# Kernel tuning notes

Measured on AMD Instinct MI355X. Metric: run time of the kernel, lower is better.

The kernel has to match this reference:

```python
import jax, jax.numpy as jnp
import numpy as np

N = 100_000      # nodes
M = 200_000      # hyperedges
E = 1_000_000    # incidence pairs
D_IN = 64
HEADS, D_OUT = 8, 16   # linear out = 8*16 = 128


def setup_inputs() -> dict:
    key = jax.random.key(0)
    k = jax.random.split(key, 7)
    X = jax.random.normal(k[0], (N, D_IN), dtype=jnp.float32)
    vertex = jax.random.randint(k[1], (E,), 0, N, dtype=jnp.int32)
    edges = jax.random.randint(k[2], (E,), 0, M, dtype=jnp.int32)
    dege = jax.random.uniform(k[3], (M, 1), dtype=jnp.float32)
    degv = jax.random.uniform(k[4], (N, 1), dtype=jnp.float32)
    W = jax.random.normal(k[5], (D_IN, HEADS * D_OUT), dtype=jnp.float32) / np.sqrt(D_IN)
    b = jax.random.normal(k[6], (HEADS * D_OUT,), dtype=jnp.float32) * 0.01
    return {"X": X, "vertex": vertex, "edges": edges, "dege": dege, "degv": degv, "W": W, "b": b}


def reference(X, vertex, edges, dege, degv, W, b):
    n_nodes = X.shape[0]
    n_edges = dege.shape[0]
    # vertex -> hyperedge aggregation (first_aggregate = 'mean')
    Xve = X[vertex]                                               # [E, D]
    sums = jax.ops.segment_sum(Xve, edges, num_segments=n_edges)  # [M, D]
    counts = jax.ops.segment_sum(jnp.ones((edges.shape[0],), X.dtype), edges, num_segments=n_edges)
    Xe = sums / jnp.maximum(counts, 1.0)[:, None]                 # empty edges -> 0
    Xe = Xe * dege
    # hyperedge -> vertex aggregation (sum)
    Xev = Xe[edges]                                               # [E, D]
    Xv = jax.ops.segment_sum(Xev, vertex, num_segments=n_nodes)   # [N, D]
    Xv = Xv * degv
    # normalize_l2: row norm is computed on a DETACHED tensor in torch
    rownorm = jnp.linalg.norm(jax.lax.stop_gradient(Xv), axis=1, keepdims=True)
    scale = jnp.where(rownorm > 0, 1.0 / rownorm, 0.0)
    Xn = Xv * scale
    return Xn @ W + b
```

## Files before the change

### kernel.cpp

```cpp
#include <hip/hip_runtime.h>


#define DIN 64
#define DOUT 128
#define CH 4096
#define BSHIFT 9
#define FINE 512
#define PAYBITS 18
#define PAYMASK ((1u << PAYBITS) - 1u)
#define XB 256
#define STAGE 8192

typedef float f32x4 __attribute__((ext_vector_type(4)));
typedef short bf16x8 __attribute__((ext_vector_type(8)));

__device__ __forceinline__ unsigned short f2b(float f) {
  unsigned u = __float_as_uint(f);
  u = u + 0x7fffu + ((u >> 16) & 1u);
  return (unsigned short)(u >> 16);
}
__device__ __forceinline__ float b2f(unsigned s) {
  return __uint_as_float(s << 16);
}

__global__ __launch_bounds__(512) void k_p1(
    const int* __restrict__ vertex, const int* __restrict__ edges,
    int* __restrict__ G, const float* __restrict__ X,
    unsigned short* __restrict__ Xb, int* __restrict__ done,
    int E, int BKE, int BK, int NCH, int total4) {
  if (blockIdx.x == 0 && threadIdx.x == 0) *done = 0;
  if (blockIdx.x >= (unsigned)NCH) {
    int xb = blockIdx.x - NCH;
    for (int i = xb * 512 + threadIdx.x; i < total4; i += XB * 512) {
      float4 a = ((const float4*)X)[i];
      ushort4 r;
      r.x = f2b(a.x); r.y = f2b(a.y); r.z = f2b(a.z); r.w = f2b(a.w);
      ((ushort4*)Xb)[i] = r;
    }
    return;
  }
  __shared__ int h[1024];
  for (int i = threadIdx.x; i < BK; i += 512) h[i] = 0;
  __syncthreads();
  int c = blockIdx.x;
  int s = c * CH, e_ = min(E, s + CH);
  int n4 = (e_ - s) >> 2;
  const int4* ep = (const int4*)(edges + s);
  const int4* vp = (const int4*)(vertex + s);
  for (int i = threadIdx.x; i < n4; i += 512) {
    int4 ee = ep[i], vv = vp[i];
    atomicAdd(&h[ee.x >> BSHIFT], 1); atomicAdd(&h[ee.y >> BSHIFT], 1);
    atomicAdd(&h[ee.z >> BSHIFT], 1); atomicAdd(&h[ee.w >> BSHIFT], 1);
    atomicAdd(&h[BKE + (vv.x >> BSHIFT)], 1); atomicAdd(&h[BKE + (vv.y >> BSHIFT)], 1);
    atomicAdd(&h[BKE + (vv.z >> BSHIFT)], 1); atomicAdd(&h[BKE + (vv.w >> BSHIFT)], 1);
  }
  for (int i = s + (n4 << 2) + threadIdx.x; i < e_; i += 512) {
    atomicAdd(&h[edges[i] >> BSHIFT], 1);
    atomicAdd(&h[BKE + (vertex[i] >> BSHIFT)], 1);
  }
  __syncthreads();
  for (int b = threadIdx.x; b < BK; b += 512) G[(size_t)b * NCH + c] = h[b];
}

__global__ __launch_bounds__(256) void k_p1b(
    int* __restrict__ G, int* __restrict__ rowTot, int* __restrict__ bucketBase,
    int* __restrict__ done, int NCH, int BK) {
  int b = blockIdx.x;
  int* row = G + (size_t)b * NCH;
  __shared__ int wsum[4];
  __shared__ int carry;
  __shared__ bool amLast;
  if (threadIdx.x == 0) carry = 0;
  __syncthreads();
  for (int base = 0; base < NCH; base += 256) {
    int i = base + threadIdx.x;
    int v = (i < NCH) ? row[i] : 0;
    int lane = threadIdx.x & 63, wid = threadIdx.x >> 6;
    int inc = v;
    #pragma unroll
    for (int o = 1; o < 64; o <<= 1) {
      int t = __shfl_up(inc, o);
      if (lane >= o) inc += t;
    }
    if (lane == 63) wsum[wid] = inc;
    __syncthreads();
    int woff = carry;
    for (int w = 0; w < wid; ++w) woff += wsum[w];
    int excl = woff + inc - v;
    if (i < NCH) row[i] = excl;
    __syncthreads();
    if (threadIdx.x == 0) carry += wsum[0] + wsum[1] + wsum[2] + wsum[3];
    __syncthreads();
  }
  if (threadIdx.x == 0) {
    rowTot[b] = carry;
    __threadfence();
    amLast = (atomicAdd(done, 1) == gridDim.x - 1);
  }
  __syncthreads();
  if (!amLast) return;

  if (threadIdx.x == 0) carry = 0;
  __syncthreads();
  for (int base = 0; base < BK; base += 256) {
    int i = base + threadIdx.x;
    int v = (i < BK) ? atomicAdd(&rowTot[i], 0) : 0;
    int lane = threadIdx.x & 63, wid = threadIdx.x >> 6;
    int inc = v;
    #pragma unroll
    for (int o = 1; o < 64; o <<= 1) {
      int t = __shfl_up(inc, o);
      if (lane >= o) inc += t;
    }
    if (lane == 63) wsum[wid] = inc;
    __syncthreads();
    int woff = carry;
    for (int w = 0; w < wid; ++w) woff += wsum[w];
    int excl = woff + inc - v;
    if (i < BK) bucketBase[i] = excl;
    __syncthreads();
    if (threadIdx.x == 0) carry += wsum[0] + wsum[1] + wsum[2] + wsum[3];
    __syncthreads();
  }
  if (threadIdx.x == 0) bucketBase[BK] = carry;
}

__global__ __launch_bounds__(512) void p2_scatter(
    const int* __restrict__ vertex, const int* __restrict__ edges,
    const int* __restrict__ G, const int* __restrict__ bucketBase,
    unsigned* __restrict__ temp, int E, int BKE, int BK, int NCH) {
  __shared__ int curs[1024];
  int c = blockIdx.x;
  for (int b = threadIdx.x; b < BK; b += 512)
    curs[b] = bucketBase[b] + G[(size_t)b * NCH + c];
  __syncthreads();
  int s = c * CH, e_ = min(E, s + CH);
  int n4 = (e_ - s) >> 2;
  const int4* ep = (const int4*)(edges + s);
  const int4* vp = (const int4*)(vertex + s);
  for (int i = threadIdx.x; i < n4; i += 512) {
    int4 ee = ep[i], vv = vp[i];
    int p;
    p = atomicAdd(&curs[ee.x >> BSHIFT], 1);
    temp[p] = ((unsigned)(ee.x & (FINE - 1)) << PAYBITS) | (unsigned)vv.x;
    p = atomicAdd(&curs[BKE + (vv.x >> BSHIFT)], 1);
    temp[p] = ((unsigned)(vv.x & (FINE - 1)) << PAYBITS) | (unsigned)ee.x;
    p = atomicAdd(&curs[ee.y >> BSHIFT], 1);
    temp[p] = ((unsigned)(ee.y & (FINE - 1)) << PAYBITS) | (unsigned)vv.y;
    p = atomicAdd(&curs[BKE + (vv.y >> BSHIFT)], 1);
    temp[p] = ((unsigned)(vv.y & (FINE - 1)) << PAYBITS) | (unsigned)ee.y;
    p = atomicAdd(&curs[ee.z >> BSHIFT], 1);
    temp[p] = ((unsigned)(ee.z & (FINE - 1)) << PAYBITS) | (unsigned)vv.z;
    p = atomicAdd(&curs[BKE + (vv.z >> BSHIFT)], 1);
    temp[p] = ((unsigned)(vv.z & (FINE - 1)) << PAYBITS) | (unsigned)ee.z;
    p = atomicAdd(&curs[ee.w >> BSHIFT], 1);
    temp[p] = ((unsigned)(ee.w & (FINE - 1)) << PAYBITS) | (unsigned)vv.w;
    p = atomicAdd(&curs[BKE + (vv.w >> BSHIFT)], 1);
    temp[p] = ((unsigned)(vv.w & (FINE - 1)) << PAYBITS) | (unsigned)ee.w;
  }
  for (int i = s + (n4 << 2) + threadIdx.x; i < e_; i += 512) {
    int e = edges[i], v = vertex[i];
    int pE = atomicAdd(&curs[e >> BSHIFT], 1);
    temp[pE] = ((unsigned)(e & (FINE - 1)) << PAYBITS) | (unsigned)v;
    int pV = atomicAdd(&curs[BKE + (v >> BSHIFT)], 1);
    temp[pV] = ((unsigned)(v & (FINE - 1)) << PAYBITS) | (unsigned)e;
  }
}

__global__ __launch_bounds__(256) void p3_sort(
    const unsigned* __restrict__ temp, const int* __restrict__ bucketBase,
    int* __restrict__ off, int* __restrict__ perm, int BKE, int M, int N) {
  __shared__ int hist[FINE];
  __shared__ int pos[FINE];
  __shared__ int wsum[4];
  __shared__ unsigned pairsS[STAGE];
  int g = blockIdx.x;
  bool isE = g < BKE;
  int gg = isE ? g : g - BKE;
  int keyBase = gg << BSHIFT;
  int cap = isE ? M : N;
  int offBase = (isE ? 0 : M) + keyBase;
  int fineCount = min(FINE, cap - keyBase);
  int pairBase = bucketBase[g], pairEnd = bucketBase[g + 1];
  int cnt = pairEnd - pairBase;
  bool staged = cnt <= STAGE;

  for (int i = threadIdx.x; i < FINE; i += 256) hist[i] = 0;
  __syncthreads();
  if (staged) {
    for (int i = threadIdx.x; i < cnt; i += 256) {
      unsigned p = temp[pairBase + i];
      pairsS[i] = p;
      atomicAdd(&hist[p >> PAYBITS], 1);
    }
  } else {
    for (int i = threadIdx.x; i < cnt; i += 256)
      atomicAdd(&hist[temp[pairBase + i] >> PAYBITS], 1);
  }
  __syncthreads();

  int t2 = threadIdx.x * 2;
  int a0 = hist[t2], a1 = hist[t2 + 1];
  int tsum = a0 + a1;
  int lane = threadIdx.x & 63, wid = threadIdx.x >> 6;
  int inc = tsum;
  #pragma unroll
  for (int o = 1; o < 64; o <<= 1) {
    int t = __shfl_up(inc, o);
    if (lane >= o) inc += t;
  }
  if (lane == 63) wsum[wid] = inc;
  __syncthreads();
  int woff = 0;
  for (int w = 0; w < wid; ++w) woff += wsum[w];
  int excl = woff + inc - tsum;
  pos[t2] = excl; pos[t2 + 1] = excl + a0;
  __syncthreads();

  for (int f = threadIdx.x; f < fineCount; f += 256)
    off[offBase + f] = pairBase + pos[f] + hist[f];
  for (int f = threadIdx.x; f < FINE; f += 256) pos[f] += pairBase;
  __syncthreads();

  if (staged) {
    for (int i = threadIdx.x; i < cnt; i += 256) {
      unsigned p = pairsS[i];
      int q = atomicAdd(&pos[p >> PAYBITS], 1);
      perm[q] = (int)(p & PAYMASK);
    }
  } else {
    for (int i = threadIdx.x; i < cnt; i += 256) {
      unsigned p = temp[pairBase + i];
      int q = atomicAdd(&pos[p >> PAYBITS], 1);
      perm[q] = (int)(p & PAYMASK);
    }
  }
}


__global__ __launch_bounds__(256) void k_edge(
    const unsigned short* __restrict__ Xb, const int* __restrict__ off,
    const int* __restrict__ perm, const float* __restrict__ dege,
    unsigned short* __restrict__ Xe, int M) {
  long long gid = (long long)blockIdx.x * 256 + threadIdx.x;
  int wv = (int)(gid >> 6);
  int lane = threadIdx.x & 63;
  int g = lane >> 3, li = lane & 7;
  int e = wv * 8 + g;
  bool valid = e < M;
  int start = 0, end = 0;
  if (valid) { start = e ? off[e - 1] : 0; end = off[e]; }
  int deg = end - start;
  int myidx = (valid && li < deg) ? perm[start + li] : 0;
  int jmax = min(deg, 8);
  int jw = jmax;
  jw = max(jw, __shfl_xor(jw, 8));
  jw = max(jw, __shfl_xor(jw, 16));
  jw = max(jw, __shfl_xor(jw, 32));
  const uint4* X4 = (const uint4*)Xb;
  float acc[8] = {0.f, 0.f, 0.f, 0.f, 0.f, 0.f, 0.f, 0.f};
  #pragma unroll 4
  for (int j = 0; j < jw; ++j) {
    int v0 = __shfl(myidx, (g << 3) + j);
    if (j < jmax) {
      uint4 a = X4[(size_t)v0 * 8 + li];
      acc[0] += b2f(a.x & 0xffffu); acc[1] += b2f(a.x >> 16);
      acc[2] += b2f(a.y & 0xffffu); acc[3] += b2f(a.y >> 16);
      acc[4] += b2f(a.z & 0xffffu); acc[5] += b2f(a.z >> 16);
      acc[6] += b2f(a.w & 0xffffu); acc[7] += b2f(a.w >> 16);
    }
  }
  for (int j = 8; j < deg; ++j) {
    int v0 = perm[start + j];
    uint4 a = X4[(size_t)v0 * 8 + li];
    acc[0] += b2f(a.x & 0xffffu); acc[1] += b2f(a.x >> 16);
    acc[2] += b2f(a.y & 0xffffu); acc[3] += b2f(a.y >> 16);
    acc[4] += b2f(a.z & 0xffffu); acc[5] += b2f(a.z >> 16);
    acc[6] += b2f(a.w & 0xffffu); acc[7] += b2f(a.w >> 16);
  }
  if (valid) {
    float s = dege[e] / fmaxf((float)deg, 1.0f);
    uint4 r;
    r.x = (unsigned)f2b(acc[0] * s) | ((unsigned)f2b(acc[1] * s) << 16);
    r.y = (unsigned)f2b(acc[2] * s) | ((unsigned)f2b(acc[3] * s) << 16);
    r.z = (unsigned)f2b(acc[4] * s) | ((unsigned)f2b(acc[5] * s) << 16);
    r.w = (unsigned)f2b(acc[6] * s) | ((unsigned)f2b(acc[7] * s) << 16);
    ((uint4*)Xe)[(size_t)e * 8 + li] = r;
  }
}

__global__ __launch_bounds__(256) void k_nodeagg(
    const unsigned short* __restrict__ Xe, const int* __restrict__ off,
    const int* __restrict__ perm, const float* __restrict__ degv,
    unsigned short* __restrict__ xn, int N, int M) {
  long long gid = (long long)blockIdx.x * 256 + threadIdx.x;
  int wv = (int)(gid >> 6);
  int lane = threadIdx.x & 63;
  int g = lane >> 3, li = lane & 7;
  int node = wv * 8 + g;
  bool valid = node < N;
  int start = 0, end = 0;
  if (valid) { start = off[M + node - 1]; end = off[M + node]; }
  int deg = end - start;
  int my0 = (valid && li < deg) ? perm[start + li] : 0;
  int my1 = (valid && 8 + li < deg) ? perm[start + 8 + li] : 0;
  int jmax0 = min(deg, 8);
  int jmax1 = min(max(deg - 8, 0), 8);
  int jw0 = jmax0, jw1 = jmax1;
  jw0 = max(jw0, __shfl_xor(jw0, 8)); jw1 = max(jw1, __shfl_xor(jw1, 8));
  jw0 = max(jw0, __shfl_xor(jw0, 16)); jw1 = max(jw1, __shfl_xor(jw1, 16));
  jw0 = max(jw0, __shfl_xor(jw0, 32)); jw1 = max(jw1, __shfl_xor(jw1, 32));
  const uint4* Xe4 = (const uint4*)Xe;
  float acc[8] = {0.f, 0.f, 0.f, 0.f, 0.f, 0.f, 0.f, 0.f};
  #pragma unroll 4
  for (int j = 0; j < jw0; ++j) {
    int e0 = __shfl(my0, (g << 3) + j);
    if (j < jmax0) {
      uint4 a = Xe4[(size_t)e0 * 8 + li];
      acc[0] += b2f(a.x & 0xffffu); acc[1] += b2f(a.x >> 16);
      acc[2] += b2f(a.y & 0xffffu); acc[3] += b2f(a.y >> 16);
      acc[4] += b2f(a.z & 0xffffu); acc[5] += b2f(a.z >> 16);
      acc[6] += b2f(a.w & 0xffffu); acc[7] += b2f(a.w >> 16);
    }
  }
  #pragma unroll 4
  for (int j = 0; j < jw1; ++j) {
    int e0 = __shfl(my1, (g << 3) + j);
    if (j < jmax1) {
      uint4 a = Xe4[(size_t)e0 * 8 + li];
      acc[0] += b2f(a.x & 0xffffu); acc[1] += b2f(a.x >> 16);
      acc[2] += b2f(a.y & 0xffffu); acc[3] += b2f(a.y >> 16);
      acc[4] += b2f(a.z & 0xffffu); acc[5] += b2f(a.z >> 16);
      acc[6] += b2f(a.w & 0xffffu); acc[7] += b2f(a.w >> 16);
    }
  }
  for (int j = 16; j < deg; ++j) {
    int e0 = perm[start + j];
    uint4 a = Xe4[(size_t)e0 * 8 + li];
    acc[0] += b2f(a.x & 0xffffu); acc[1] += b2f(a.x >> 16);
    acc[2] += b2f(a.y & 0xffffu); acc[3] += b2f(a.y >> 16);
    acc[4] += b2f(a.z & 0xffffu); acc[5] += b2f(a.z >> 16);
    acc[6] += b2f(a.w & 0xffffu); acc[7] += b2f(a.w >> 16);
  }
  float dv = valid ? degv[node] : 0.f;
  float ss = 0.f;
  #pragma unroll
  for (int i = 0; i < 8; ++i) { acc[i] *= dv; ss += acc[i] * acc[i]; }
  #pragma unroll
  for (int o = 1; o <= 4; o <<= 1) ss += __shfl_xor(ss, o);
  float sc = ss > 0.0f ? 1.0f / sqrtf(ss) : 0.0f;
  if (valid) {
    uint4 r;
    r.x = (unsigned)f2b(acc[0] * sc) | ((unsigned)f2b(acc[1] * sc) << 16);
    r.y = (unsigned)f2b(acc[2] * sc) | ((unsigned)f2b(acc[3] * sc) << 16);
    r.z = (unsigned)f2b(acc[4] * sc) | ((unsigned)f2b(acc[5] * sc) << 16);
    r.w = (unsigned)f2b(acc[6] * sc) | ((unsigned)f2b(acc[7] * sc) << 16);
    ((uint4*)xn)[(size_t)node * 8 + li] = r;
  }
}

#define WPAD 72
__global__ __launch_bounds__(256) void k_linear(
    const unsigned short* __restrict__ xn, const float* __restrict__ W,
    const float* __restrict__ bias, float* __restrict__ out, int N) {
  __shared__ unsigned short Wt[DOUT * WPAD];
  for (int i = threadIdx.x; i < DIN * DOUT; i += 256) {
    int k = i >> 7, c = i & 127;
    Wt[c * WPAD + k] = f2b(W[i]);
  }
  __syncthreads();
  int lane = threadIdx.x & 63;
  int wid = threadIdx.x >> 6;
  int r = lane & 15, h = lane >> 4;

  bf16x8 Bf[8][2];
  #pragma unroll
  for (int c = 0; c < 8; ++c) {
    #pragma unroll
    for (int ks = 0; ks < 2; ++ks) {
      int col = c * 16 + r;
      int k0 = ks * 32 + h * 8;
      Bf[c][ks] = *(const bf16x8*)&Wt[col * WPAD + k0];
    }
  }
  float bcol[8];
  #pragma unroll
  for (int c = 0; c < 8; ++c) bcol[c] = bias[c * 16 + r];

  int strips = (N + 15) >> 4;
  for (int s = blockIdx.x * 4 + wid; s < strips; s += gridDim.x * 4) {
    int row0 = s << 4;
    const unsigned short* xrow = xn + (size_t)(row0 + r) * DIN;
    bf16x8 a0 = *(const bf16x8*)&xrow[h * 8];
    bf16x8 a1 = *(const bf16x8*)&xrow[32 + h * 8];
    #pragma unroll
    for (int c = 0; c < 8; ++c) {
      f32x4 acc = {bcol[c], bcol[c], bcol[c], bcol[c]};
      acc = __builtin_amdgcn_mfma_f32_16x16x32_bf16(a0, Bf[c][0], acc, 0, 0, 0);
      acc = __builtin_amdgcn_mfma_f32_16x16x32_bf16(a1, Bf[c][1], acc, 0, 0, 0);
      #pragma unroll
      for (int q = 0; q < 4; ++q)
        out[(size_t)(row0 + h * 4 + q) * DOUT + c * 16 + r] = acc[q];
    }
  }
}

extern "C" void kernel_launch(void* const* d_in, const int* in_sizes, int n_in,
                              void* d_out, int out_size, void* d_ws, size_t ws_size,
                              hipStream_t stream) {
  const float* X      = (const float*)d_in[0];
  const int*   vertex = (const int*)d_in[1];
  const int*   edges  = (const int*)d_in[2];
  const float* dege   = (const float*)d_in[3];
  const float* degv   = (const float*)d_in[4];
  const float* W      = (const float*)d_in[5];
  const float* b      = (const float*)d_in[6];
  float* out = (float*)d_out;

  int N = in_sizes[0] / DIN;
  int E = in_sizes[1];
  int M = in_sizes[3];

  int NCH = (E + CH - 1) / CH;
  int BKE = (M + FINE - 1) >> BSHIFT;
  int BKV = (N + FINE - 1) >> BSHIFT;
  int BK  = BKE + BKV;

  unsigned short* Xe = (unsigned short*)d_ws;
  unsigned short* Xb = Xe + (size_t)M * DIN;
  int*   off  = (int*)(Xb + (size_t)N * DIN);
  int*   perm = off + (M + N);
  char*  R    = (char*)(perm + 2 * (size_t)E);
  unsigned*       temp = (unsigned*)R;
  unsigned short* xn   = (unsigned short*)R;
  size_t rBytes = (size_t)2 * E * 4;
  size_t xBytes = (size_t)N * DIN * 2;
  char*  R2   = R + (rBytes > xBytes ? rBytes : xBytes);
  int*   G    = (int*)R2;
  int*   rowTot = G + (size_t)BK * NCH;
  int*   bucketBase = rowTot + BK;
  int*   done = bucketBase + BK + 1;

  int total4 = N * DIN / 4;
  k_p1<<<NCH + XB, 512, 0, stream>>>(vertex, edges, G, X, Xb, done,
                                     E, BKE, BK, NCH, total4);
  k_p1b<<<BK, 256, 0, stream>>>(G, rowTot, bucketBase, done, NCH, BK);
  p2_scatter<<<NCH, 512, 0, stream>>>(vertex, edges, G, bucketBase, temp,
                                      E, BKE, BK, NCH);
  p3_sort<<<BK, 256, 0, stream>>>(temp, bucketBase, off, perm, BKE, M, N);

  int edgeBlocks = (M + 31) / 32;
  k_edge<<<edgeBlocks, 256, 0, stream>>>(Xb, off, perm, dege, Xe, M);

  int nodeWaves = (N + 7) / 8;
  int nodeBlocks = (nodeWaves + 3) / 4;
  k_nodeagg<<<nodeBlocks, 256, 0, stream>>>(Xe, off, perm, degv, xn, N, M);

  int strips = (N + 15) >> 4;
  int linBlocks = (strips + 3) / 4;
  k_linear<<<linBlocks, 256, 0, stream>>>(xn, W, b, out, N);
}
```

Baseline: 130.4 us.

## Fuse node aggregation, L2 normalization and linear projection into one kernel

Measured after the change: 132.1 us. About the same (+1.3%).

```diff
diff --git a/kernel.cpp b/kernel.cpp
--- a/kernel.cpp
+++ b/kernel.cpp
@@ -10,6 +10,7 @@
 #define PAYMASK ((1u << PAYBITS) - 1u)
 #define XB 256
 #define STAGE 8192
+#define WPAD 72
 
 typedef float f32x4 __attribute__((ext_vector_type(4)));
 typedef short bf16x8 __attribute__((ext_vector_type(8)));
@@ -289,118 +290,120 @@
   }
 }
 
-__global__ __launch_bounds__(256) void k_nodeagg(
+__global__ __launch_bounds__(256) void k_nodefin(
     const unsigned short* __restrict__ Xe, const int* __restrict__ off,
     const int* __restrict__ perm, const float* __restrict__ degv,
-    unsigned short* __restrict__ xn, int N, int M) {
-  long long gid = (long long)blockIdx.x * 256 + threadIdx.x;
-  int wv = (int)(gid >> 6);
-  int lane = threadIdx.x & 63;
-  int g = lane >> 3, li = lane & 7;
-  int node = wv * 8 + g;
-  bool valid = node < N;
-  int start = 0, end = 0;
-  if (valid) { start = off[M + node - 1]; end = off[M + node]; }
-  int deg = end - start;
-  int my0 = (valid && li < deg) ? perm[start + li] : 0;
-  int my1 = (valid && 8 + li < deg) ? perm[start + 8 + li] : 0;
-  int jmax0 = min(deg, 8);
-  int jmax1 = min(max(deg - 8, 0), 8);
-  int jw0 = jmax0, jw1 = jmax1;
-  jw0 = max(jw0, __shfl_xor(jw0, 8)); jw1 = max(jw1, __shfl_xor(jw1, 8));
-  jw0 = max(jw0, __shfl_xor(jw0, 16)); jw1 = max(jw1, __shfl_xor(jw1, 16));
-  jw0 = max(jw0, __shfl_xor(jw0, 32)); jw1 = max(jw1, __shfl_xor(jw1, 32));
-  const uint4* Xe4 = (const uint4*)Xe;
-  float acc[8] = {0.f, 0.f, 0.f, 0.f, 0.f, 0.f, 0.f, 0.f};
-  #pragma unroll 4
-  for (int j = 0; j < jw0; ++j) {
-    int e0 = __shfl(my0, (g << 3) + j);
-    if (j < jmax0) {
-      uint4 a = Xe4[(size_t)e0 * 8 + li];
-      acc[0] += b2f(a.x & 0xffffu); acc[1] += b2f(a.x >> 16);
-      acc[2] += b2f(a.y & 0xffffu); acc[3] += b2f(a.y >> 16);
-      acc[4] += b2f(a.z & 0xffffu); acc[5] += b2f(a.z >> 16);
-      acc[6] += b2f(a.w & 0xffffu); acc[7] += b2f(a.w >> 16);
-    }
-  }
-  #pragma unroll 4
-  for (int j = 0; j < jw1; ++j) {
-    int e0 = __shfl(my1, (g << 3) + j);
-    if (j < jmax1) {
-      uint4 a = Xe4[(size_t)e0 * 8 + li];
-      acc[0] += b2f(a.x & 0xffffu); acc[1] += b2f(a.x >> 16);
-      acc[2] += b2f(a.y & 0xffffu); acc[3] += b2f(a.y >> 16);
-      acc[4] += b2f(a.z & 0xffffu); acc[5] += b2f(a.z >> 16);
-      acc[6] += b2f(a.w & 0xffffu); acc[7] += b2f(a.w >> 16);
-    }
-  }
-  for (int j = 16; j < deg; ++j) {
-    int e0 = perm[start + j];
-    uint4 a = Xe4[(size_t)e0 * 8 + li];
-    acc[0] += b2f(a.x & 0xffffu); acc[1] += b2f(a.x >> 16);
-    acc[2] += b2f(a.y & 0xffffu); acc[3] += b2f(a.y >> 16);
-    acc[4] += b2f(a.z & 0xffffu); acc[5] += b2f(a.z >> 16);
-    acc[6] += b2f(a.w & 0xffffu); acc[7] += b2f(a.w >> 16);
-  }
-  float dv = valid ? degv[node] : 0.f;
-  float ss = 0.f;
-  #pragma unroll
-  for (int i = 0; i < 8; ++i) { acc[i] *= dv; ss += acc[i] * acc[i]; }
-  #pragma unroll
-  for (int o = 1; o <= 4; o <<= 1) ss += __shfl_xor(ss, o);
-  float sc = ss > 0.0f ? 1.0f / sqrtf(ss) : 0.0f;
-  if (valid) {
-    uint4 r;
-    r.x = (unsigned)f2b(acc[0] * sc) | ((unsigned)f2b(acc[1] * sc) << 16);
-    r.y = (unsigned)f2b(acc[2] * sc) | ((unsigned)f2b(acc[3] * sc) << 16);
-    r.z = (unsigned)f2b(acc[4] * sc) | ((unsigned)f2b(acc[5] * sc) << 16);
-    r.w = (unsigned)f2b(acc[6] * sc) | ((unsigned)f2b(acc[7] * sc) << 16);
-    ((uint4*)xn)[(size_t)node * 8 + li] = r;
-  }
-}
-
-#define WPAD 72
-__global__ __launch_bounds__(256) void k_linear(
-    const unsigned short* __restrict__ xn, const float* __restrict__ W,
-    const float* __restrict__ bias, float* __restrict__ out, int N) {
+    const float* __restrict__ W, const float* __restrict__ bias,
+    float* __restrict__ out, int N, int M) {
   __shared__ unsigned short Wt[DOUT * WPAD];
+  __shared__ __align__(16) unsigned short xnS[4][16][WPAD];
   for (int i = threadIdx.x; i < DIN * DOUT; i += 256) {
     int k = i >> 7, c = i & 127;
     Wt[c * WPAD + k] = f2b(W[i]);
   }
   __syncthreads();
+
+  int wv = threadIdx.x >> 6;
   int lane = threadIdx.x & 63;
-  int wid = threadIdx.x >> 6;
+  int g = lane >> 3, li = lane & 7;
+  int row0 = (blockIdx.x * 4 + wv) * 16;
+  int nA = row0 + g;
+  int nB = row0 + 8 + g;
+  bool vA = nA < N, vB = nB < N;
+  int sA = 0, eA = 0, sB = 0, eB = 0;
+  if (vA) { sA = off[M + nA - 1]; eA = off[M + nA]; }
+  if (vB) { sB = off[M + nB - 1]; eB = off[M + nB]; }
+  int dA = eA - sA, dB = eB - sB;
+  int myA0 = (vA && li < dA) ? perm[sA + li] : 0;
+  int myA1 = (vA && 8 + li < dA) ? perm[sA + 8 + li] : 0;
+  int myB0 = (vB && li < dB) ? perm[sB + li] : 0;
+  int myB1 = (vB && 8 + li < dB) ? perm[sB + 8 + li] : 0;
+  int jA = min(dA, 16), jB = min(dB, 16);
+  int jw = max(jA, jB);
+  jw = max(jw, __shfl_xor(jw, 8));
+  jw = max(jw, __shfl_xor(jw, 16));
+  jw = max(jw, __shfl_xor(jw, 32));
+  const uint4* Xe4 = (const uint4*)Xe;
+  float accA[8] = {0.f, 0.f, 0.f, 0.f, 0.f, 0.f, 0.f, 0.f};
+  float accB[8] = {0.f, 0.f, 0.f, 0.f, 0.f, 0.f, 0.f, 0.f};
+  #pragma unroll 2
+  for (int j = 0; j < jw; ++j) {
+    int iA = (j < 8) ? __shfl(myA0, (g << 3) + j) : __shfl(myA1, (g << 3) + j - 8);
+    int iB = (j < 8) ? __shfl(myB0, (g << 3) + j) : __shfl(myB1, (g << 3) + j - 8);
+    if (j < jA) {
+      uint4 a = Xe4[(size_t)iA * 8 + li];
+      accA[0] += b2f(a.x & 0xffffu); accA[1] += b2f(a.x >> 16);
+      accA[2] += b2f(a.y & 0xffffu); accA[3] += b2f(a.y >> 16);
+      accA[4] += b2f(a.z & 0xffffu); accA[5] += b2f(a.z >> 16);
+      accA[6] += b2f(a.w & 0xffffu); accA[7] += b2f(a.w >> 16);
+    }
+    if (j < jB) {
+      uint4 a = Xe4[(size_t)iB * 8 + li];
+      accB[0] += b2f(a.x & 0xffffu); accB[1] += b2f(a.x >> 16);
+      accB[2] += b2f(a.y & 0xffffu); accB[3] += b2f(a.y >> 16);
+      accB[4] += b2f(a.z & 0xffffu); accB[5] += b2f(a.z >> 16);
+      accB[6] += b2f(a.w & 0xffffu); accB[7] += b2f(a.w >> 16);
+    }
+  }
+  for (int j = 16; j < dA; ++j) {
+    int e0 = perm[sA + j];
+    uint4 a = Xe4[(size_t)e0 * 8 + li];
+    accA[0] += b2f(a.x & 0xffffu); accA[1] += b2f(a.x >> 16);
+    accA[2] += b2f(a.y & 0xffffu); accA[3] += b2f(a.y >> 16);
+    accA[4] += b2f(a.z & 0xffffu); accA[5] += b2f(a.z >> 16);
+    accA[6] += b2f(a.w & 0xffffu); accA[7] += b2f(a.w >> 16);
+  }
+  for (int j = 16; j < dB; ++j) {
+    int e0 = perm[sB + j];
+    uint4 a = Xe4[(size_t)e0 * 8 + li];
+    accB[0] += b2f(a.x & 0xffffu); accB[1] += b2f(a.x >> 16);
+    accB[2] += b2f(a.y & 0xffffu); accB[3] += b2f(a.y >> 16);
+    accB[4] += b2f(a.z & 0xffffu); accB[5] += b2f(a.z >> 16);
+    accB[6] += b2f(a.w & 0xffffu); accB[7] += b2f(a.w >> 16);
+  }
+  float dvA = vA ? degv[nA] : 0.f;
+  float dvB = vB ? degv[nB] : 0.f;
+  float ssA = 0.f, ssB = 0.f;
+  #pragma unroll
+  for (int i = 0; i < 8; ++i) {
+    accA[i] *= dvA; ssA += accA[i] * accA[i];
+    accB[i] *= dvB; ssB += accB[i] * accB[i];
+  }
+  #pragma unroll
+  for (int o = 1; o <= 4; o <<= 1) {
+    ssA += __shfl_xor(ssA, o);
+    ssB += __shfl_xor(ssB, o);
+  }
+  float scA = ssA > 0.0f ? 1.0f / sqrtf(ssA) : 0.0f;
+  float scB = ssB > 0.0f ? 1.0f / sqrtf(ssB) : 0.0f;
+  uint4 rA, rB;
+  rA.x = (unsigned)f2b(accA[0] * scA) | ((unsigned)f2b(accA[1] * scA) << 16);
+  rA.y = (unsigned)f2b(accA[2] * scA) | ((unsigned)f2b(accA[3] * scA) << 16);
+  rA.z = (unsigned)f2b(accA[4] * scA) | ((unsigned)f2b(accA[5] * scA) << 16);
+  rA.w = (unsigned)f2b(accA[6] * scA) | ((unsigned)f2b(accA[7] * scA) << 16);
+  rB.x = (unsigned)f2b(accB[0] * scB) | ((unsigned)f2b(accB[1] * scB) << 16);
+  rB.y = (unsigned)f2b(accB[2] * scB) | ((unsigned)f2b(accB[3] * scB) << 16);
+  rB.z = (unsigned)f2b(accB[4] * scB) | ((unsigned)f2b(accB[5] * scB) << 16);
+  rB.w = (unsigned)f2b(accB[6] * scB) | ((unsigned)f2b(accB[7] * scB) << 16);
+  *(uint4*)&xnS[wv][g][li * 8] = rA;
+  *(uint4*)&xnS[wv][8 + g][li * 8] = rB;
+
   int r = lane & 15, h = lane >> 4;
-
-  bf16x8 Bf[8][2];
+  bf16x8 a0 = *(const bf16x8*)&xnS[wv][r][h * 8];
+  bf16x8 a1 = *(const bf16x8*)&xnS[wv][r][32 + h * 8];
   #pragma unroll
   for (int c = 0; c < 8; ++c) {
+    const unsigned short* wcol = &Wt[(c * 16 + r) * WPAD];
+    bf16x8 b0 = *(const bf16x8*)&wcol[h * 8];
+    bf16x8 b1 = *(const bf16x8*)&wcol[32 + h * 8];
+    float bc = bias[c * 16 + r];
+    f32x4 o4 = {bc, bc, bc, bc};
+    o4 = __builtin_amdgcn_mfma_f32_16x16x32_bf16(a0, b0, o4, 0, 0, 0);
+    o4 = __builtin_amdgcn_mfma_f32_16x16x32_bf16(a1, b1, o4, 0, 0, 0);
     #pragma unroll
-    for (int ks = 0; ks < 2; ++ks) {
-      int col = c * 16 + r;
-      int k0 = ks * 32 + h * 8;
-      Bf[c][ks] = *(const bf16x8*)&Wt[col * WPAD + k0];
-    }
-  }
-  float bcol[8];
-  #pragma unroll
-  for (int c = 0; c < 8; ++c) bcol[c] = bias[c * 16 + r];
-
-  int strips = (N + 15) >> 4;
-  for (int s = blockIdx.x * 4 + wid; s < strips; s += gridDim.x * 4) {
-    int row0 = s << 4;
-    const unsigned short* xrow = xn + (size_t)(row0 + r) * DIN;
-    bf16x8 a0 = *(const bf16x8*)&xrow[h * 8];
-    bf16x8 a1 = *(const bf16x8*)&xrow[32 + h * 8];
-    #pragma unroll
-    for (int c = 0; c < 8; ++c) {
-      f32x4 acc = {bcol[c], bcol[c], bcol[c], bcol[c]};
-      acc = __builtin_amdgcn_mfma_f32_16x16x32_bf16(a0, Bf[c][0], acc, 0, 0, 0);
-      acc = __builtin_amdgcn_mfma_f32_16x16x32_bf16(a1, Bf[c][1], acc, 0, 0, 0);
-      #pragma unroll
-      for (int q = 0; q < 4; ++q)
-        out[(size_t)(row0 + h * 4 + q) * DOUT + c * 16 + r] = acc[q];
+    for (int q = 0; q < 4; ++q) {
+      int row = row0 + h * 4 + q;
+      if (row < N) out[(size_t)row * DOUT + c * 16 + r] = o4[q];
     }
   }
 }
@@ -430,13 +433,8 @@
   unsigned short* Xb = Xe + (size_t)M * DIN;
   int*   off  = (int*)(Xb + (size_t)N * DIN);
   int*   perm = off + (M + N);
-  char*  R    = (char*)(perm + 2 * (size_t)E);
-  unsigned*       temp = (unsigned*)R;
-  unsigned short* xn   = (unsigned short*)R;
-  size_t rBytes = (size_t)2 * E * 4;
-  size_t xBytes = (size_t)N * DIN * 2;
-  char*  R2   = R + (rBytes > xBytes ? rBytes : xBytes);
-  int*   G    = (int*)R2;
+  unsigned* temp = (unsigned*)(perm + 2 * (size_t)E);
+  int*   G    = (int*)(temp + 2 * (size_t)E);
   int*   rowTot = G + (size_t)BK * NCH;
   int*   bucketBase = rowTot + BK;
   int*   done = bucketBase + BK + 1;
@@ -452,11 +450,7 @@
   int edgeBlocks = (M + 31) / 32;
   k_edge<<<edgeBlocks, 256, 0, stream>>>(Xb, off, perm, dege, Xe, M);
 
-  int nodeWaves = (N + 7) / 8;
-  int nodeBlocks = (nodeWaves + 3) / 4;
-  k_nodeagg<<<nodeBlocks, 256, 0, stream>>>(Xe, off, perm, degv, xn, N, M);
-
-  int strips = (N + 15) >> 4;
-  int linBlocks = (strips + 3) / 4;
-  k_linear<<<linBlocks, 256, 0, stream>>>(xn, W, b, out, N);
-}
+  int nodeBlocks = (N + 63) / 64;
+  k_nodefin<<<nodeBlocks, 256, 0, stream>>>(Xe, off, perm, degv, W, b,
+                                            out, N, M);
+}
```
